# Performance work log

Measured on AMD Instinct MI355X. Metric: run time of the kernel, lower is better.

## Reference

```python
import jax, jax.numpy as jnp
import numpy as np

BN_EPS = 1e-5
L2_EPS = 1e-12


def _gconv(x, adj, W, b):
    # x: [B, N, F_in], adj: [N, N] (densified sparse), W: [F_in, F_out]
    y = jnp.einsum('rc,bcf->brf', adj, x)          # sparse aggregation (spmm)
    y = jnp.einsum('brf,fo->bro', y, W) + b        # dense transform + bias
    n = jnp.sqrt(jnp.sum(y * y, axis=2, keepdims=True))
    return y / jnp.maximum(n, L2_EPS)              # F.normalize(p=2, dim=2)


def _bn3(x):
    # BatchNorm1d over channel dim=1 (roinum), batch stats, affine = identity
    m = jnp.mean(x, axis=(0, 2), keepdims=True)
    v = jnp.var(x, axis=(0, 2), keepdims=True)
    return (x - m) / jnp.sqrt(v + BN_EPS)


def _bn2(x):
    m = jnp.mean(x, axis=0, keepdims=True)
    v = jnp.var(x, axis=0, keepdims=True)
    return (x - m) / jnp.sqrt(v + BN_EPS)


def setup_inputs() -> dict:
    key = jax.random.key(0)
    ks = jax.random.split(key, 20)
    B, N, F_in, H, E, L = 256, 400, 400, 64, 64, 2
    NNZ = 16000
    pred_in = H * 2 + E  # hidden*(num_layers-1) + embedding = 192
    nhid = H

    def xavier(k, fi, fo):
        s = np.sqrt(6.0 / (fi + fo))
        return jax.random.uniform(k, (fi, fo), jnp.float32, -s, s)

    return {
        'x': jax.random.normal(ks[0], (B, N, F_in), jnp.float32),
        'adj_rows': jax.random.randint(ks[1], (NNZ,), 0, N, jnp.int32),
        'adj_cols': jax.random.randint(ks[2], (NNZ,), 0, N, jnp.int32),
        'adj_vals': jax.random.uniform(ks[3], (NNZ,), jnp.float32),
        'W1': xavier(ks[4], F_in, H), 'b1': jnp.zeros((H,), jnp.float32),
        'W2': xavier(ks[5], H, H),    'b2': jnp.zeros((H,), jnp.float32),
        'W3': xavier(ks[6], H, E),    'b3': jnp.zeros((E,), jnp.float32),
        'fc1_W': xavier(ks[7], pred_in, nhid), 'fc1_b': jnp.zeros((nhid,), jnp.float32),
        'fc2_W': xavier(ks[8], nhid, nhid),    'fc2_b': jnp.zeros((nhid,), jnp.float32),
        'fc3_W': xavier(ks[9], nhid, L),       'fc3_b': jnp.zeros((L,), jnp.float32),
    }


def reference(x, adj_rows, adj_cols, adj_vals,
              W1, b1, W2, b2, W3, b3,
              fc1_W, fc1_b, fc2_W, fc2_b, fc3_W, fc3_b):
    N = x.shape[1]
    adj = jnp.zeros((N, N), x.dtype).at[adj_rows, adj_cols].add(adj_vals)

    x1 = _bn3(jax.nn.relu(_gconv(x, adj, W1, b1)))
    out1 = jnp.max(x1, axis=1)                     # [B, H]
    x2 = _bn3(jax.nn.relu(_gconv(x1, adj, W2, b2)))
    out2 = jnp.max(x2, axis=1)                     # [B, H]
    x3 = _gconv(x2, adj, W3, b3)                   # [B, N, E]
    out3 = jnp.max(x3, axis=1)                     # [B, E]

    h = jnp.concatenate([out1, out2, out3], axis=1)  # [B, 2H+E]
    h = _bn2(jax.nn.relu(h @ fc1_W + fc1_b))
    h = _bn2(jax.nn.relu(h @ fc2_W + fc2_b))
    ypred = h @ fc3_W + fc3_b
    return ypred, x3
```

## Files before the change

### kernel.cpp

```cpp
#include <hip/hip_runtime.h>
#include <hip/hip_bf16.h>
#include <math.h>

#define Bb   256
#define Nn   400
#define FIN  400
#define Hh   64
#define NNZ  16000
#define Mrows (Bb*Nn)
#define KP   416
#define UTP  416
#define BH_COUNT 16384.0f

typedef unsigned int  u32x2 __attribute__((ext_vector_type(2)));
typedef unsigned int  u32x4 __attribute__((ext_vector_type(4)));
typedef __bf16        bf16x8 __attribute__((ext_vector_type(8)));
typedef float         f32x4 __attribute__((ext_vector_type(4)));

__device__ __forceinline__ unsigned int f2bf(float x) {
    unsigned int u = __builtin_bit_cast(unsigned int, x);
    return (u + 0x7FFFu + ((u >> 16) & 1u)) >> 16;
}
__device__ __forceinline__ float bf2f(unsigned int h) {
    unsigned int u = h << 16;
    return __builtin_bit_cast(float, u);
}

__global__ void initk(float* __restrict__ Adf, float* __restrict__ stats,
                      unsigned short* __restrict__ Ut) {
    int t = blockIdx.x * blockDim.x + threadIdx.x;
    if (t < Nn * KP) Adf[t] = 0.f;
    if (t < 1600) stats[t] = 0.f;
    if (t < Bb * Hh * 16) {
        int bh = t >> 4, k = Nn + (t & 15);
        Ut[(size_t)bh * UTP + k] = 0;
    }
}

__global__ void scatAk(const int* __restrict__ rows, const int* __restrict__ cols,
                       const float* __restrict__ vals, float* __restrict__ Adf) {
    int i = blockIdx.x * blockDim.x + threadIdx.x;
    if (i < NNZ) atomicAdd(&Adf[rows[i] * KP + cols[i]], vals[i]);
}

__global__ void cvtAk(const float* __restrict__ Adf, unsigned short* __restrict__ Adbf) {
    int i = blockIdx.x * blockDim.x + threadIdx.x;
    if (i < Nn * KP) Adbf[i] = (unsigned short)f2bf(Adf[i]);
}

__global__ __launch_bounds__(256) void wprep(
        const float* __restrict__ W1, const float* __restrict__ W2,
        const float* __restrict__ W3,
        unsigned short* __restrict__ T1h, unsigned short* __restrict__ T1l,
        unsigned short* __restrict__ T2h, unsigned short* __restrict__ T2l,
        unsigned short* __restrict__ T3h, unsigned short* __restrict__ T3l,
        float* __restrict__ cs2, float* __restrict__ cs3) {
    const int w = blockIdx.x >> 6;
    const int c = blockIdx.x & 63;
    const float* W = (w == 0) ? W1 : (w == 1) ? W2 : W3;
    const int KT   = (w == 0) ? FIN : Hh;
    const int KPAD = (w == 0) ? 416 : 64;
    unsigned short* Th = (w == 0) ? T1h : (w == 1) ? T2h : T3h;
    unsigned short* Tl = (w == 0) ? T1l : (w == 1) ? T2l : T3l;

    float s = 0.f;
    for (int k = threadIdx.x; k < KPAD; k += 256) {
        float v = (k < KT) ? W[k * 64 + c] : 0.f;
        unsigned int hb = f2bf(v);
        Th[c * KPAD + k] = (unsigned short)hb;
        Tl[c * KPAD + k] = (unsigned short)f2bf(v - bf2f(hb));
        s += v;
    }
    __shared__ float red[256];
    red[threadIdx.x] = s;
    __syncthreads();
    for (int o = 128; o; o >>= 1) {
        if (threadIdx.x < o) red[threadIdx.x] += red[threadIdx.x + o];
        __syncthreads();
    }
    if (threadIdx.x == 0) {
        if (w == 1) cs2[c] = red[0];
        else if (w == 2) cs3[c] = red[0];
    }
}

__global__ __launch_bounds__(256) void xg400(
        const float* __restrict__ A,
        const unsigned short* __restrict__ Wth,
        const unsigned short* __restrict__ Wtl,
        unsigned short* __restrict__ Ut) {
    const int tid  = threadIdx.x;
    const int wv   = tid >> 6;
    const int lane = tid & 63;
    const int cl   = lane & 15;
    const int g    = lane >> 4;
    const int m0   = blockIdx.x * 128;
    const int rowA = m0 + wv * 32 + cl;
    const int rowB = rowA + 16;

    f32x4 acc[2][4];
#pragma unroll
    for (int t2 = 0; t2 < 2; ++t2)
#pragma unroll
        for (int n = 0; n < 4; ++n) acc[t2][n] = f32x4{0.f, 0.f, 0.f, 0.f};

    auto loadA = [&](int s, float4& l0, float4& h0, float4& l1, float4& h1) {
        int kk = s * 32 + g * 8;
        int kc = kk > 392 ? 392 : kk;
        const float* p = &A[(size_t)rowA * FIN + kc];
        l0 = *reinterpret_cast<const float4*>(p);
        h0 = *reinterpret_cast<const float4*>(p + 4);
        const float* q = &A[(size_t)rowB * FIN + kc];
        l1 = *reinterpret_cast<const float4*>(q);
        h1 = *reinterpret_cast<const float4*>(q + 4);
    };
    auto loadW = [&](int s, u32x4* dst) {
        int kk = s * 32 + g * 8;
#pragma unroll
        for (int n = 0; n < 4; ++n) {
            dst[n]     = *reinterpret_cast<const u32x4*>(&Wth[(size_t)(n * 16 + cl) * 416 + kk]);
            dst[4 + n] = *reinterpret_cast<const u32x4*>(&Wtl[(size_t)(n * 16 + cl) * 416 + kk]);
        }
    };
    auto split = [&](const float4& lo, const float4& hi, bf16x8& ah, bf16x8& al) {
        float v0 = lo.x, v1 = lo.y, v2 = lo.z, v3 = lo.w;
        float v4 = hi.x, v5 = hi.y, v6 = hi.z, v7 = hi.w;
        unsigned h0, h1;
        u32x4 hw, lw;
        h0 = f2bf(v0); h1 = f2bf(v1);
        hw[0] = h0 | (h1 << 16);
        lw[0] = f2bf(v0 - bf2f(h0)) | (f2bf(v1 - bf2f(h1)) << 16);
        h0 = f2bf(v2); h1 = f2bf(v3);
        hw[1] = h0 | (h1 << 16);
        lw[1] = f2bf(v2 - bf2f(h0)) | (f2bf(v3 - bf2f(h1)) << 16);
        h0 = f2bf(v4); h1 = f2bf(v5);
        hw[2] = h0 | (h1 << 16);
        lw[2] = f2bf(v4 - bf2f(h0)) | (f2bf(v5 - bf2f(h1)) << 16);
        h0 = f2bf(v6); h1 = f2bf(v7);
        hw[3] = h0 | (h1 << 16);
        lw[3] = f2bf(v6 - bf2f(h0)) | (f2bf(v7 - bf2f(h1)) << 16);
        ah = __builtin_bit_cast(bf16x8, hw);
        al = __builtin_bit_cast(bf16x8, lw);
    };

    float4 cAl0, cAh0, cAl1, cAh1, nAl0, nAh0, nAl1, nAh1;
    u32x4  cW[8], nW[8];
    loadA(0, cAl0, cAh0, cAl1, cAh1);
    loadW(0, cW);

    for (int s = 0; s < 13; ++s) {
        if (s < 12) {
            loadA(s + 1, nAl0, nAh0, nAl1, nAh1);
            loadW(s + 1, nW);
        }
        bf16x8 ah0, al0, ah1, al1;
        split(cAl0, cAh0, ah0, al0);
        split(cAl1, cAh1, ah1, al1);
#pragma unroll
        for (int n = 0; n < 4; ++n) {
            bf16x8 bh = __builtin_bit_cast(bf16x8, cW[n]);
            bf16x8 bl = __builtin_bit_cast(bf16x8, cW[4 + n]);
            acc[0][n] = __builtin_amdgcn_mfma_f32_16x16x32_bf16(ah0, bh, acc[0][n], 0, 0, 0);
            acc[0][n] = __builtin_amdgcn_mfma_f32_16x16x32_bf16(ah0, bl, acc[0][n], 0, 0, 0);
            acc[0][n] = __builtin_amdgcn_mfma_f32_16x16x32_bf16(al0, bh, acc[0][n], 0, 0, 0);
            acc[1][n] = __builtin_amdgcn_mfma_f32_16x16x32_bf16(ah1, bh, acc[1][n], 0, 0, 0);
            acc[1][n] = __builtin_amdgcn_mfma_f32_16x16x32_bf16(ah1, bl, acc[1][n], 0, 0, 0);
            acc[1][n] = __builtin_amdgcn_mfma_f32_16x16x32_bf16(al1, bh, acc[1][n], 0, 0, 0);
        }
        if (s < 12) {
            cAl0 = nAl0; cAh0 = nAh0; cAl1 = nAl1; cAh1 = nAh1;
#pragma unroll
            for (int j = 0; j < 8; ++j) cW[j] = nW[j];
        }
    }

#pragma unroll
    for (int t2 = 0; t2 < 2; ++t2) {
        const int row0  = m0 + wv * 32 + t2 * 16 + g * 4;
        const int b     = row0 / Nn;
        const int node0 = row0 - b * Nn;
#pragma unroll
        for (int n = 0; n < 4; ++n) {
            const int col = n * 16 + cl;
            u32x2 pk;
            pk[0] = f2bf(acc[t2][n][0]) | (f2bf(acc[t2][n][1]) << 16);
            pk[1] = f2bf(acc[t2][n][2]) | (f2bf(acc[t2][n][3]) << 16);
            *reinterpret_cast<u32x2*>(&Ut[((size_t)b * 64 + col) * UTP + node0]) = pk;
        }
    }
}

__global__ __launch_bounds__(256) void xg64(
        const float* __restrict__ A,
        const unsigned short* __restrict__ Wth,
        const unsigned short* __restrict__ Wtl,
        const float* __restrict__ csW,
        unsigned short* __restrict__ Ut,
        const float* __restrict__ mean, const float* __restrict__ inv) {
    const int tid  = threadIdx.x;
    const int wv   = tid >> 6;
    const int lane = tid & 63;
    const int cl   = lane & 15;
    const int g    = lane >> 4;
    const int m0   = blockIdx.x * 64;
    const int arow = m0 + wv * 16 + cl;

    f32x4 acc[4];
#pragma unroll
    for (int n = 0; n < 4; ++n) acc[n] = f32x4{0.f, 0.f, 0.f, 0.f};

#pragma unroll
    for (int s = 0; s < 2; ++s) {
        const int kk = s * 32 + g * 8;
        const float* p = &A[(size_t)arow * 64 + kk];
        float4 lo = *reinterpret_cast<const float4*>(p);
        float4 hi = *reinterpret_cast<const float4*>(p + 4);
        float av[8] = {lo.x, lo.y, lo.z, lo.w, hi.x, hi.y, hi.z, hi.w};
        u32x4 ahw, alw;
#pragma unroll
        for (int j = 0; j < 4; ++j) {
            unsigned int h0 = f2bf(av[2 * j]);
            unsigned int h1 = f2bf(av[2 * j + 1]);
            unsigned int l0 = f2bf(av[2 * j]     - bf2f(h0));
            unsigned int l1 = f2bf(av[2 * j + 1] - bf2f(h1));
            ahw[j] = h0 | (h1 << 16);
            alw[j] = l0 | (l1 << 16);
        }
        bf16x8 ah = __builtin_bit_cast(bf16x8, ahw);
        bf16x8 al = __builtin_bit_cast(bf16x8, alw);
#pragma unroll
        for (int n = 0; n < 4; ++n) {
            u32x4 bhw = *reinterpret_cast<const u32x4*>(&Wth[(size_t)(n * 16 + cl) * 64 + kk]);
            u32x4 blw = *reinterpret_cast<const u32x4*>(&Wtl[(size_t)(n * 16 + cl) * 64 + kk]);
            bf16x8 bh = __builtin_bit_cast(bf16x8, bhw);
            bf16x8 bl = __builtin_bit_cast(bf16x8, blw);
            acc[n] = __builtin_amdgcn_mfma_f32_16x16x32_bf16(ah, bh, acc[n], 0, 0, 0);
            acc[n] = __builtin_amdgcn_mfma_f32_16x16x32_bf16(ah, bl, acc[n], 0, 0, 0);
            acc[n] = __builtin_amdgcn_mfma_f32_16x16x32_bf16(al, bh, acc[n], 0, 0, 0);
        }
    }

    const int row0  = m0 + wv * 16 + g * 4;
    const int b     = row0 / Nn;
    const int node0 = row0 - b * Nn;
    float mm[4], iv[4];
#pragma unroll
    for (int r = 0; r < 4; ++r) { mm[r] = mean[node0 + r]; iv[r] = inv[node0 + r]; }
#pragma unroll
    for (int n = 0; n < 4; ++n) {
        const int col = n * 16 + cl;
        const float cw = csW[col];
        float y[4];
#pragma unroll
        for (int r = 0; r < 4; ++r)
            y[r] = iv[r] * (acc[n][r] - mm[r] * cw);
        u32x2 pk;
        pk[0] = f2bf(y[0]) | (f2bf(y[1]) << 16);
        pk[1] = f2bf(y[2]) | (f2bf(y[3]) << 16);
        *reinterpret_cast<u32x2*>(&Ut[((size_t)b * 64 + col) * UTP + node0]) = pk;
    }
}

template <bool STATS>
__global__ __launch_bounds__(256) void aggmm(
        const unsigned short* __restrict__ Ad,
        const unsigned short* __restrict__ Ut,
        const float* __restrict__ bias,
        float* __restrict__ Zout,
        float* __restrict__ ssum, float* __restrict__ ssq) {
    const int b    = blockIdx.x >> 2;
    const int q    = blockIdx.x & 3;
    const int tid  = threadIdx.x;
    const int lane = tid & 63;
    const int wv   = tid >> 6;
    const int cl   = lane & 15;
    const int g    = lane >> 4;
    const unsigned short* __restrict__ Ub = Ut + (size_t)b * 64 * UTP;

    f32x4 acc[2][4];
#pragma unroll
    for (int i = 0; i < 2; ++i)
#pragma unroll
        for (int n = 0; n < 4; ++n) acc[i][n] = f32x4{0.f, 0.f, 0.f, 0.f};

    for (int k0 = 0; k0 < KP; k0 += 32) {
        const int kk = k0 + g * 8;
        bf16x8 bf[4];
#pragma unroll
        for (int n = 0; n < 4; ++n) {
            u32x4 w = *reinterpret_cast<const u32x4*>(&Ub[(size_t)(n * 16 + cl) * UTP + kk]);
            bf[n] = __builtin_bit_cast(bf16x8, w);
        }
#pragma unroll
        for (int i = 0; i < 2; ++i) {
            const int t = q + 4 * wv + 16 * i;
            if (t < 25) {
                const int row = t * 16 + cl;
                u32x4 ar = *reinterpret_cast<const u32x4*>(&Ad[(size_t)row * KP + kk]);
                bf16x8 af = __builtin_bit_cast(bf16x8, ar);
#pragma unroll
                for (int n = 0; n < 4; ++n)
                    acc[i][n] = __builtin_amdgcn_mfma_f32_16x16x32_bf16(
                        af, bf[n], acc[i][n], 0, 0, 0);
            }
        }
    }

    float bv[4];
#pragma unroll
    for (int n = 0; n < 4; ++n) bv[n] = bias[n * 16 + cl];

#pragma unroll
    for (int i = 0; i < 2; ++i) {
        const int t = q + 4 * wv + 16 * i;
        if (t < 25) {
            float y[4][4];
#pragma unroll
            for (int n = 0; n < 4; ++n)
#pragma unroll
                for (int r = 0; r < 4; ++r) y[n][r] = acc[i][n][r] + bv[n];

            float pss[4];
#pragma unroll
            for (int r = 0; r < 4; ++r)
                pss[r] = y[0][r]*y[0][r] + y[1][r]*y[1][r] +
                         y[2][r]*y[2][r] + y[3][r]*y[3][r];
#pragma unroll
            for (int m = 1; m < 16; m <<= 1)
#pragma unroll
                for (int r = 0; r < 4; ++r) pss[r] += __shfl_xor(pss[r], m);

            float rin[4];
#pragma unroll
            for (int r = 0; r < 4; ++r)
                rin[r] = 1.f / fmaxf(sqrtf(pss[r]), 1e-12f);

#pragma unroll
            for (int n = 0; n < 4; ++n)
#pragma unroll
                for (int r = 0; r < 4; ++r) {
                    float z = y[n][r] * rin[r];
                    if (STATS) z = fmaxf(z, 0.f);
                    y[n][r] = z;
                    const int row = t * 16 + g * 4 + r;
                    Zout[((size_t)b * Nn + row) * Hh + n * 16 + cl] = z;
                }

            if (STATS) {
                float s1[4], s2[4];
#pragma unroll
                for (int r = 0; r < 4; ++r) {
                    s1[r] = y[0][r] + y[1][r] + y[2][r] + y[3][r];
                    s2[r] = y[0][r]*y[0][r] + y[1][r]*y[1][r] +
                            y[2][r]*y[2][r] + y[3][r]*y[3][r];
                }
#pragma unroll
                for (int m = 1; m < 16; m <<= 1)
#pragma unroll
                    for (int r = 0; r < 4; ++r) {
                        s1[r] += __shfl_xor(s1[r], m);
                        s2[r] += __shfl_xor(s2[r], m);
                    }
                if (cl == 0) {
#pragma unroll
                    for (int r = 0; r < 4; ++r) {
                        const int row = t * 16 + g * 4 + r;
                        atomicAdd(&ssum[row], s1[r]);
                        atomicAdd(&ssq[row],  s2[r]);
                    }
                }
            }
        }
    }
}

__global__ void finalize_stats(const float* __restrict__ ssum,
                               const float* __restrict__ ssq,
                               float* __restrict__ mean, float* __restrict__ inv) {
    int r = threadIdx.x;
    if (r < Nn) {
        float m = ssum[r] * (1.0f / BH_COUNT);
        float v = ssq[r] * (1.0f / BH_COUNT) - m * m;
        mean[r] = m;
        inv[r]  = rsqrtf(v + 1e-5f);
    }
}

template <bool AFF>
__global__ __launch_bounds__(256) void maxk(
        const float* __restrict__ Z, const float* __restrict__ mean,
        const float* __restrict__ inv, float* __restrict__ out) {
    __shared__ float red[4][64];
    const int b  = blockIdx.x;
    const int h  = threadIdx.x & 63;
    const int rg = threadIdx.x >> 6;
    float best = -3.4e38f;
    for (int r = rg; r < Nn; r += 4) {
        float v = Z[((size_t)b * Nn + r) * Hh + h];
        if (AFF) v = (v - mean[r]) * inv[r];
        best = fmaxf(best, v);
    }
    red[rg][h] = best;
    __syncthreads();
    if (threadIdx.x < 64) {
        float m = fmaxf(fmaxf(red[0][threadIdx.x], red[1][threadIdx.x]),
                        fmaxf(red[2][threadIdx.x], red[3][threadIdx.x]));
        out[b * Hh + threadIdx.x] = m;
    }
}

__global__ __launch_bounds__(1024) void headk(
        const float* __restrict__ out1, const float* __restrict__ out2,
        const float* __restrict__ out3,
        const float* __restrict__ W1f, const float* __restrict__ b1f,
        const float* __restrict__ W2f, const float* __restrict__ b2f,
        const float* __restrict__ W3f, const float* __restrict__ b3f,
        float* __restrict__ ypred) {
    __shared__ float gA[256][64];
    __shared__ float w1s[192 * 64];
    __shared__ float w2s[64 * 64];
    __shared__ float mS[64], iS[64];
    const int t = threadIdx.x;
    const int r = t >> 2, q = t & 3;

    for (int i = t; i < 192 * 64; i += 1024) w1s[i] = W1f[i];
    for (int i = t; i < 64 * 64; i += 1024) w2s[i] = W2f[i];
    __syncthreads();

    float acc[16];
#pragma unroll
    for (int j = 0; j < 16; ++j) acc[j] = b1f[q * 16 + j];
    for (int k = 0; k < 192; ++k) {
        float hv = (k < 64) ? out1[r * 64 + k]
                 : (k < 128) ? out2[r * 64 + (k - 64)]
                             : out3[r * 64 + (k - 128)];
#pragma unroll
        for (int j = 0; j < 16; ++j) acc[j] += hv * w1s[k * 64 + q * 16 + j];
    }
#pragma unroll
    for (int j = 0; j < 16; ++j) gA[r][q * 16 + j] = fmaxf(acc[j], 0.f);
    __syncthreads();

    if (t < 64) {
        float s = 0.f, s2 = 0.f;
        for (int rr = 0; rr < 256; ++rr) { float v = gA[rr][t]; s += v; s2 += v * v; }
        float m = s * (1.f / 256.f);
        float var = s2 * (1.f / 256.f) - m * m;
        mS[t] = m;
        iS[t] = rsqrtf(var + 1e-5f);
    }
    __syncthreads();

#pragma unroll
    for (int j = 0; j < 16; ++j) acc[j] = b2f[q * 16 + j];
#pragma unroll
    for (int k = 0; k < 64; ++k) {
        float gn = (gA[r][k] - mS[k]) * iS[k];
#pragma unroll
        for (int j = 0; j < 16; ++j) acc[j] += gn * w2s[k * 64 + q * 16 + j];
    }
    __syncthreads();
#pragma unroll
    for (int j = 0; j < 16; ++j) gA[r][q * 16 + j] = fmaxf(acc[j], 0.f);
    __syncthreads();

    if (t < 64) {
        float s = 0.f, s2 = 0.f;
        for (int rr = 0; rr < 256; ++rr) { float v = gA[rr][t]; s += v; s2 += v * v; }
        float m = s * (1.f / 256.f);
        float var = s2 * (1.f / 256.f) - m * m;
        mS[t] = m;
        iS[t] = rsqrtf(var + 1e-5f);
    }
    __syncthreads();

    if (q < 2) {
        float a = b3f[q];
#pragma unroll
        for (int k = 0; k < 64; ++k) {
            float gn = (gA[r][k] - mS[k]) * iS[k];
            a += gn * W3f[k * 2 + q];
        }
        ypred[r * 2 + q] = a;
    }
}

extern "C" void kernel_launch(void* const* d_in, const int* in_sizes, int n_in,
                              void* d_out, int out_size, void* d_ws, size_t ws_size,
                              hipStream_t stream) {
    const float* x    = (const float*)d_in[0];
    const int*   arow = (const int*)d_in[1];
    const int*   acol = (const int*)d_in[2];
    const float* aval = (const float*)d_in[3];
    const float* W1 = (const float*)d_in[4];
    const float* b1 = (const float*)d_in[5];
    const float* W2 = (const float*)d_in[6];
    const float* b2 = (const float*)d_in[7];
    const float* W3 = (const float*)d_in[8];
    const float* b3 = (const float*)d_in[9];
    const float* fc1W = (const float*)d_in[10];
    const float* fc1b = (const float*)d_in[11];
    const float* fc2W = (const float*)d_in[12];
    const float* fc2b = (const float*)d_in[13];
    const float* fc3W = (const float*)d_in[14];
    const float* fc3b = (const float*)d_in[15];

    char* w = (char*)d_ws;
    size_t off = 0;
    float* Adf = (float*)(w + off);            off += (size_t)Nn * KP * 4;
    unsigned short* Adbf = (unsigned short*)(w + off); off += (size_t)Nn * KP * 2;
    unsigned short* T1h = (unsigned short*)(w + off); off += (size_t)64 * 416 * 2;
    unsigned short* T1l = (unsigned short*)(w + off); off += (size_t)64 * 416 * 2;
    unsigned short* T2h = (unsigned short*)(w + off); off += (size_t)64 * 64 * 2;
    unsigned short* T2l = (unsigned short*)(w + off); off += (size_t)64 * 64 * 2;
    unsigned short* T3h = (unsigned short*)(w + off); off += (size_t)64 * 64 * 2;
    unsigned short* T3l = (unsigned short*)(w + off); off += (size_t)64 * 64 * 2;
    float* cs2 = (float*)(w + off); off += 64 * 4;
    float* cs3 = (float*)(w + off); off += 64 * 4;
    unsigned short* Ut = (unsigned short*)(w + off); off += (size_t)Bb * 64 * UTP * 2;
    float* Z = (float*)(w + off);              off += (size_t)Mrows * Hh * 4;
    float* stats = (float*)(w + off);          off += 1600 * 4;
    float* ssum1 = stats, *ssq1 = stats + 400, *ssum2 = stats + 800, *ssq2 = stats + 1200;
    float* mean1 = (float*)(w + off); off += 1600;
    float* inv1  = (float*)(w + off); off += 1600;
    float* mean2 = (float*)(w + off); off += 1600;
    float* inv2  = (float*)(w + off); off += 1600;
    float* out1  = (float*)(w + off); off += Bb * Hh * 4;
    float* out2  = (float*)(w + off); off += Bb * Hh * 4;
    float* out3  = (float*)(w + off); off += Bb * Hh * 4;

    float* ypred = (float*)d_out;
    float* x3    = (float*)d_out + 512;

    initk<<<384, 1024, 0, stream>>>(Adf, stats, Ut);
    scatAk<<<(NNZ + 255) / 256, 256, 0, stream>>>(arow, acol, aval, Adf);
    cvtAk<<<(Nn * KP + 1023) / 1024, 1024, 0, stream>>>(Adf, Adbf);
    wprep<<<192, 256, 0, stream>>>(W1, W2, W3, T1h, T1l, T2h, T2l, T3h, T3l, cs2, cs3);

    xg400<<<Mrows / 128, 256, 0, stream>>>(x, T1h, T1l, Ut);
    aggmm<true><<<Bb * 4, 256, 0, stream>>>(Adbf, Ut, b1, Z, ssum1, ssq1);
    finalize_stats<<<1, 512, 0, stream>>>(ssum1, ssq1, mean1, inv1);
    maxk<true><<<Bb, 256, 0, stream>>>(Z, mean1, inv1, out1);

    xg64<<<Mrows / 64, 256, 0, stream>>>(Z, T2h, T2l, cs2, Ut, mean1, inv1);
    aggmm<true><<<Bb * 4, 256, 0, stream>>>(Adbf, Ut, b2, Z, ssum2, ssq2);
    finalize_stats<<<1, 512, 0, stream>>>(ssum2, ssq2, mean2, inv2);
    maxk<true><<<Bb, 256, 0, stream>>>(Z, mean2, inv2, out2);

    xg64<<<Mrows / 64, 256, 0, stream>>>(Z, T3h, T3l, cs3, Ut, mean2, inv2);
    aggmm<false><<<Bb * 4, 256, 0, stream>>>(Adbf, Ut, b3, x3, nullptr, nullptr);
    maxk<false><<<Bb, 256, 0, stream>>>(x3, nullptr, nullptr, out3);

    headk<<<1, 1024, 0, stream>>>(out1, out2, out3, fc1W, fc1b, fc2W, fc2b,
                                  fc3W, fc3b, ypred);
}
```

Before: 377.8 us.

## Fuse per-node max pooling into the feature transform and aggregation kernels

The separate maxk passes that re-read Z are removed. The BN-normalised max for layers one and two is now computed inside a new per-batch transform kernel (xgb), which also applies the normalisation before the bf16 split instead of folding it via weight column sums. The layer-three max is taken inside aggmm as per-block partial maxima, which a small red4max kernel then combines. This cuts roughly two full reads of the Z/x3 tensors and a few launches, but xgb runs only 256 blocks, which may lower occupancy compared with the previous 1600-block grid.

```diff
diff --git a/kernel.cpp b/kernel.cpp
--- a/kernel.cpp
+++ b/kernel.cpp
@@ -53,8 +53,7 @@
         const float* __restrict__ W3,
         unsigned short* __restrict__ T1h, unsigned short* __restrict__ T1l,
         unsigned short* __restrict__ T2h, unsigned short* __restrict__ T2l,
-        unsigned short* __restrict__ T3h, unsigned short* __restrict__ T3l,
-        float* __restrict__ cs2, float* __restrict__ cs3) {
+        unsigned short* __restrict__ T3h, unsigned short* __restrict__ T3l) {
     const int w = blockIdx.x >> 6;
     const int c = blockIdx.x & 63;
     const float* W = (w == 0) ? W1 : (w == 1) ? W2 : W3;
@@ -63,24 +62,11 @@
     unsigned short* Th = (w == 0) ? T1h : (w == 1) ? T2h : T3h;
     unsigned short* Tl = (w == 0) ? T1l : (w == 1) ? T2l : T3l;
 
-    float s = 0.f;
     for (int k = threadIdx.x; k < KPAD; k += 256) {
         float v = (k < KT) ? W[k * 64 + c] : 0.f;
         unsigned int hb = f2bf(v);
         Th[c * KPAD + k] = (unsigned short)hb;
         Tl[c * KPAD + k] = (unsigned short)f2bf(v - bf2f(hb));
-        s += v;
-    }
-    __shared__ float red[256];
-    red[threadIdx.x] = s;
-    __syncthreads();
-    for (int o = 128; o; o >>= 1) {
-        if (threadIdx.x < o) red[threadIdx.x] += red[threadIdx.x + o];
-        __syncthreads();
-    }
-    if (threadIdx.x == 0) {
-        if (w == 1) cs2[c] = red[0];
-        else if (w == 2) cs3[c] = red[0];
     }
 }
 
@@ -190,74 +176,109 @@
     }
 }
 
-__global__ __launch_bounds__(256) void xg64(
-        const float* __restrict__ A,
+__global__ __launch_bounds__(512) void xgb(
+        const float* __restrict__ Z,
         const unsigned short* __restrict__ Wth,
         const unsigned short* __restrict__ Wtl,
-        const float* __restrict__ csW,
+        const float* __restrict__ mean, const float* __restrict__ inv,
         unsigned short* __restrict__ Ut,
-        const float* __restrict__ mean, const float* __restrict__ inv) {
+        float* __restrict__ outmax) {
+    __shared__ float smax[8][64];
+    const int b    = blockIdx.x;
     const int tid  = threadIdx.x;
     const int wv   = tid >> 6;
     const int lane = tid & 63;
     const int cl   = lane & 15;
     const int g    = lane >> 4;
-    const int m0   = blockIdx.x * 64;
-    const int arow = m0 + wv * 16 + cl;
-
-    f32x4 acc[4];
-#pragma unroll
-    for (int n = 0; n < 4; ++n) acc[n] = f32x4{0.f, 0.f, 0.f, 0.f};
-
-#pragma unroll
-    for (int s = 0; s < 2; ++s) {
-        const int kk = s * 32 + g * 8;
-        const float* p = &A[(size_t)arow * 64 + kk];
-        float4 lo = *reinterpret_cast<const float4*>(p);
-        float4 hi = *reinterpret_cast<const float4*>(p + 4);
-        float av[8] = {lo.x, lo.y, lo.z, lo.w, hi.x, hi.y, hi.z, hi.w};
-        u32x4 ahw, alw;
-#pragma unroll
-        for (int j = 0; j < 4; ++j) {
-            unsigned int h0 = f2bf(av[2 * j]);
-            unsigned int h1 = f2bf(av[2 * j + 1]);
-            unsigned int l0 = f2bf(av[2 * j]     - bf2f(h0));
-            unsigned int l1 = f2bf(av[2 * j + 1] - bf2f(h1));
-            ahw[j] = h0 | (h1 << 16);
-            alw[j] = l0 | (l1 << 16);
-        }
-        bf16x8 ah = __builtin_bit_cast(bf16x8, ahw);
-        bf16x8 al = __builtin_bit_cast(bf16x8, alw);
-#pragma unroll
-        for (int n = 0; n < 4; ++n) {
-            u32x4 bhw = *reinterpret_cast<const u32x4*>(&Wth[(size_t)(n * 16 + cl) * 64 + kk]);
-            u32x4 blw = *reinterpret_cast<const u32x4*>(&Wtl[(size_t)(n * 16 + cl) * 64 + kk]);
-            bf16x8 bh = __builtin_bit_cast(bf16x8, bhw);
-            bf16x8 bl = __builtin_bit_cast(bf16x8, blw);
-            acc[n] = __builtin_amdgcn_mfma_f32_16x16x32_bf16(ah, bh, acc[n], 0, 0, 0);
-            acc[n] = __builtin_amdgcn_mfma_f32_16x16x32_bf16(ah, bl, acc[n], 0, 0, 0);
-            acc[n] = __builtin_amdgcn_mfma_f32_16x16x32_bf16(al, bh, acc[n], 0, 0, 0);
-        }
-    }
-
-    const int row0  = m0 + wv * 16 + g * 4;
-    const int b     = row0 / Nn;
-    const int node0 = row0 - b * Nn;
-    float mm[4], iv[4];
-#pragma unroll
-    for (int r = 0; r < 4; ++r) { mm[r] = mean[node0 + r]; iv[r] = inv[node0 + r]; }
-#pragma unroll
-    for (int n = 0; n < 4; ++n) {
-        const int col = n * 16 + cl;
-        const float cw = csW[col];
-        float y[4];
-#pragma unroll
-        for (int r = 0; r < 4; ++r)
-            y[r] = iv[r] * (acc[n][r] - mm[r] * cw);
-        u32x2 pk;
-        pk[0] = f2bf(y[0]) | (f2bf(y[1]) << 16);
-        pk[1] = f2bf(y[2]) | (f2bf(y[3]) << 16);
-        *reinterpret_cast<u32x2*>(&Ut[((size_t)b * 64 + col) * UTP + node0]) = pk;
+
+    float vmax[16];
+#pragma unroll
+    for (int j = 0; j < 16; ++j) vmax[j] = -3.4e38f;
+
+    for (int i = 0; i < 4; ++i) {
+        const int t = wv + 8 * i;
+        if (t < 25) {
+            const int node = t * 16 + cl;
+            const float mm = mean[node], iv = inv[node];
+
+            float za[16];
+#pragma unroll
+            for (int s = 0; s < 2; ++s) {
+                const float* p = &Z[((size_t)b * Nn + node) * 64 + s * 32 + g * 8];
+                float4 lo = *reinterpret_cast<const float4*>(p);
+                float4 hi = *reinterpret_cast<const float4*>(p + 4);
+                za[s * 8 + 0] = (lo.x - mm) * iv;
+                za[s * 8 + 1] = (lo.y - mm) * iv;
+                za[s * 8 + 2] = (lo.z - mm) * iv;
+                za[s * 8 + 3] = (lo.w - mm) * iv;
+                za[s * 8 + 4] = (hi.x - mm) * iv;
+                za[s * 8 + 5] = (hi.y - mm) * iv;
+                za[s * 8 + 6] = (hi.z - mm) * iv;
+                za[s * 8 + 7] = (hi.w - mm) * iv;
+            }
+#pragma unroll
+            for (int j = 0; j < 16; ++j) vmax[j] = fmaxf(vmax[j], za[j]);
+
+            f32x4 acc[4];
+#pragma unroll
+            for (int n = 0; n < 4; ++n) acc[n] = f32x4{0.f, 0.f, 0.f, 0.f};
+
+#pragma unroll
+            for (int s = 0; s < 2; ++s) {
+                u32x4 hw, lw;
+#pragma unroll
+                for (int j = 0; j < 4; ++j) {
+                    unsigned h0 = f2bf(za[s * 8 + 2 * j]);
+                    unsigned h1 = f2bf(za[s * 8 + 2 * j + 1]);
+                    hw[j] = h0 | (h1 << 16);
+                    lw[j] = f2bf(za[s * 8 + 2 * j] - bf2f(h0)) |
+                            (f2bf(za[s * 8 + 2 * j + 1] - bf2f(h1)) << 16);
+                }
+                bf16x8 ah = __builtin_bit_cast(bf16x8, hw);
+                bf16x8 al = __builtin_bit_cast(bf16x8, lw);
+                const int kk = s * 32 + g * 8;
+#pragma unroll
+                for (int n = 0; n < 4; ++n) {
+                    u32x4 bhw = *reinterpret_cast<const u32x4*>(&Wth[(size_t)(n * 16 + cl) * 64 + kk]);
+                    u32x4 blw = *reinterpret_cast<const u32x4*>(&Wtl[(size_t)(n * 16 + cl) * 64 + kk]);
+                    bf16x8 bh = __builtin_bit_cast(bf16x8, bhw);
+                    bf16x8 bl = __builtin_bit_cast(bf16x8, blw);
+                    acc[n] = __builtin_amdgcn_mfma_f32_16x16x32_bf16(ah, bh, acc[n], 0, 0, 0);
+                    acc[n] = __builtin_amdgcn_mfma_f32_16x16x32_bf16(ah, bl, acc[n], 0, 0, 0);
+                    acc[n] = __builtin_amdgcn_mfma_f32_16x16x32_bf16(al, bh, acc[n], 0, 0, 0);
+                }
+            }
+
+            const int node0 = t * 16 + g * 4;
+#pragma unroll
+            for (int n = 0; n < 4; ++n) {
+                const int col = n * 16 + cl;
+                u32x2 pk;
+                pk[0] = f2bf(acc[n][0]) | (f2bf(acc[n][1]) << 16);
+                pk[1] = f2bf(acc[n][2]) | (f2bf(acc[n][3]) << 16);
+                *reinterpret_cast<u32x2*>(&Ut[((size_t)b * 64 + col) * UTP + node0]) = pk;
+            }
+        }
+    }
+
+#pragma unroll
+    for (int m = 1; m < 16; m <<= 1)
+#pragma unroll
+        for (int j = 0; j < 16; ++j)
+            vmax[j] = fmaxf(vmax[j], __shfl_xor(vmax[j], m));
+    if (cl == 0) {
+#pragma unroll
+        for (int j = 0; j < 16; ++j) {
+            const int h = 32 * (j >> 3) + g * 8 + (j & 7);
+            smax[wv][h] = vmax[j];
+        }
+    }
+    __syncthreads();
+    if (tid < 64) {
+        float m = smax[0][tid];
+#pragma unroll
+        for (int w = 1; w < 8; ++w) m = fmaxf(m, smax[w][tid]);
+        outmax[b * 64 + tid] = m;
     }
 }
 
@@ -267,7 +288,8 @@
         const unsigned short* __restrict__ Ut,
         const float* __restrict__ bias,
         float* __restrict__ Zout,
-        float* __restrict__ ssum, float* __restrict__ ssq) {
+        float* __restrict__ ssum, float* __restrict__ ssq,
+        float* __restrict__ pmaxq) {
     const int b    = blockIdx.x >> 2;
     const int q    = blockIdx.x & 3;
     const int tid  = threadIdx.x;
@@ -310,6 +332,10 @@
 #pragma unroll
     for (int n = 0; n < 4; ++n) bv[n] = bias[n * 16 + cl];
 
+    float pmax[4];
+#pragma unroll
+    for (int n = 0; n < 4; ++n) pmax[n] = -3.4e38f;
+
 #pragma unroll
     for (int i = 0; i < 2; ++i) {
         const int t = q + 4 * wv + 16 * i;
@@ -344,6 +370,7 @@
                     y[n][r] = z;
                     const int row = t * 16 + g * 4 + r;
                     Zout[((size_t)b * Nn + row) * Hh + n * 16 + cl] = z;
+                    if (!STATS) pmax[n] = fmaxf(pmax[n], z);
                 }
 
             if (STATS) {
@@ -372,6 +399,34 @@
             }
         }
     }
+
+    if constexpr (!STATS) {
+        __shared__ float sm[4][64];
+#pragma unroll
+        for (int m = 16; m < 64; m <<= 1)
+#pragma unroll
+            for (int n = 0; n < 4; ++n)
+                pmax[n] = fmaxf(pmax[n], __shfl_xor(pmax[n], m));
+        if (lane < 16) {
+#pragma unroll
+            for (int n = 0; n < 4; ++n) sm[wv][n * 16 + cl] = pmax[n];
+        }
+        __syncthreads();
+        if (tid < 64) {
+            float m = fmaxf(fmaxf(sm[0][tid], sm[1][tid]),
+                            fmaxf(sm[2][tid], sm[3][tid]));
+            pmaxq[(size_t)blockIdx.x * 64 + tid] = m;
+        }
+    }
+}
+
+__global__ void red4max(const float* __restrict__ pmaxq, float* __restrict__ out3) {
+    const int b = blockIdx.x, h = threadIdx.x;
+    float m = pmaxq[(size_t)(b * 4 + 0) * 64 + h];
+    m = fmaxf(m, pmaxq[(size_t)(b * 4 + 1) * 64 + h]);
+    m = fmaxf(m, pmaxq[(size_t)(b * 4 + 2) * 64 + h]);
+    m = fmaxf(m, pmaxq[(size_t)(b * 4 + 3) * 64 + h]);
+    out3[b * 64 + h] = m;
 }
 
 __global__ void finalize_stats(const float* __restrict__ ssum,
@@ -383,29 +438,6 @@
         float v = ssq[r] * (1.0f / BH_COUNT) - m * m;
         mean[r] = m;
         inv[r]  = rsqrtf(v + 1e-5f);
-    }
-}
-
-template <bool AFF>
-__global__ __launch_bounds__(256) void maxk(
-        const float* __restrict__ Z, const float* __restrict__ mean,
-        const float* __restrict__ inv, float* __restrict__ out) {
-    __shared__ float red[4][64];
-    const int b  = blockIdx.x;
-    const int h  = threadIdx.x & 63;
-    const int rg = threadIdx.x >> 6;
-    float best = -3.4e38f;
-    for (int r = rg; r < Nn; r += 4) {
-        float v = Z[((size_t)b * Nn + r) * Hh + h];
-        if (AFF) v = (v - mean[r]) * inv[r];
-        best = fmaxf(best, v);
-    }
-    red[rg][h] = best;
-    __syncthreads();
-    if (threadIdx.x < 64) {
-        float m = fmaxf(fmaxf(red[0][threadIdx.x], red[1][threadIdx.x]),
-                        fmaxf(red[2][threadIdx.x], red[3][threadIdx.x]));
-        out[b * Hh + threadIdx.x] = m;
     }
 }
 
@@ -515,8 +547,6 @@
     unsigned short* T2l = (unsigned short*)(w + off); off += (size_t)64 * 64 * 2;
     unsigned short* T3h = (unsigned short*)(w + off); off += (size_t)64 * 64 * 2;
     unsigned short* T3l = (unsigned short*)(w + off); off += (size_t)64 * 64 * 2;
-    float* cs2 = (float*)(w + off); off += 64 * 4;
-    float* cs3 = (float*)(w + off); off += 64 * 4;
     unsigned short* Ut = (unsigned short*)(w + off); off += (size_t)Bb * 64 * UTP * 2;
     float* Z = (float*)(w + off);              off += (size_t)Mrows * Hh * 4;
     float* stats = (float*)(w + off);          off += 1600 * 4;
@@ -528,6 +558,7 @@
     float* out1  = (float*)(w + off); off += Bb * Hh * 4;
     float* out2  = (float*)(w + off); off += Bb * Hh * 4;
     float* out3  = (float*)(w + off); off += Bb * Hh * 4;
+    float* pmaxq = (float*)(w + off); off += (size_t)Bb * 4 * 64 * 4;
 
     float* ypred = (float*)d_out;
     float* x3    = (float*)d_out + 512;
@@ -535,21 +566,19 @@
     initk<<<384, 1024, 0, stream>>>(Adf, stats, Ut);
     scatAk<<<(NNZ + 255) / 256, 256, 0, stream>>>(arow, acol, aval, Adf);
     cvtAk<<<(Nn * KP + 1023) / 1024, 1024, 0, stream>>>(Adf, Adbf);
-    wprep<<<192, 256, 0, stream>>>(W1, W2, W3, T1h, T1l, T2h, T2l, T3h, T3l, cs2, cs3);
+    wprep<<<192, 256, 0, stream>>>(W1, W2, W3, T1h, T1l, T2h, T2l, T3h, T3l);
 
     xg400<<<Mrows / 128, 256, 0, stream>>>(x, T1h, T1l, Ut);
-    aggmm<true><<<Bb * 4, 256, 0, stream>>>(Adbf, Ut, b1, Z, ssum1, ssq1);
+    aggmm<true><<<Bb * 4, 256, 0, stream>>>(Adbf, Ut, b1, Z, ssum1, ssq1, nullptr);
     finalize_stats<<<1, 512, 0, stream>>>(ssum1, ssq1, mean1, inv1);
-    maxk<true><<<Bb, 256, 0, stream>>>(Z, mean1, inv1, out1);
-
-    xg64<<<Mrows / 64, 256, 0, stream>>>(Z, T2h, T2l, cs2, Ut, mean1, inv1);
-    aggmm<true><<<Bb * 4, 256, 0, stream>>>(Adbf, Ut, b2, Z, ssum2, ssq2);
+
+    xgb<<<Bb, 512, 0, stream>>>(Z, T2h, T2l, mean1, inv1, Ut, out1);
+    aggmm<true><<<Bb * 4, 256, 0, stream>>>(Adbf, Ut, b2, Z, ssum2, ssq2, nullptr);
     finalize_stats<<<1, 512, 0, stream>>>(ssum2, ssq2, mean2, inv2);
-    maxk<true><<<Bb, 256, 0, stream>>>(Z, mean2, inv2, out2);
-
-    xg64<<<Mrows / 64, 256, 0, stream>>>(Z, T3h, T3l, cs3, Ut, mean2, inv2);
-    aggmm<false><<<Bb * 4, 256, 0, stream>>>(Adbf, Ut, b3, x3, nullptr, nullptr);
-    maxk<false><<<Bb, 256, 0, stream>>>(x3, nullptr, nullptr, out3);
+
+    xgb<<<Bb, 512, 0, stream>>>(Z, T3h, T3l, mean2, inv2, Ut, out2);
+    aggmm<false><<<Bb * 4, 256, 0, stream>>>(Adbf, Ut, b3, x3, nullptr, nullptr, pmaxq);
+    red4max<<<Bb, 64, 0, stream>>>(pmaxq, out3);
 
     headk<<<1, 1024, 0, stream>>>(out1, out2, out3, fc1W, fc1b, fc2W, fc2b,
                                   fc3W, fc3b, ypred);
```

Measured after the change: 318.4 us. 15.7% less time.
